# Kernel optimization log

Hardware: AMD Instinct MI355X
Metric: run time of the kernel (lower is better)

Reference implementation:

```python
import jax, jax.numpy as jnp
import numpy as np

N, E, F_DIM = 30000, 480000, 256
CLS_HID, NUM_CLASS, GEN_HID, MI_HID, BATCH = 128, 16, 64, 128, 4096
COM_L1, COM_L2, LAM, ALPHA, TAU, EPS = 0.5, 0.5, 0.5, 1.0, 0.5, 1e-8


def _glorot(key, shape):
    scale = jnp.sqrt(2.0 / (shape[0] + shape[-1]))
    return scale * jax.random.normal(key, shape, dtype=jnp.float32)


def setup_inputs() -> dict:
    key = jax.random.key(0)
    ks = jax.random.split(key, 32)
    inp = {
        'feat': jax.random.normal(ks[0], (N, F_DIM), dtype=jnp.float32),
        'view1_indices': jax.random.randint(ks[1], (2, E), 0, N),
        'view1_values': jax.random.uniform(ks[2], (E,), dtype=jnp.float32),
        'view2_indices': jax.random.randint(ks[3], (2, E), 0, N),
        'view2_values': jax.random.uniform(ks[4], (E,), dtype=jnp.float32),
        'idx': jnp.sort(jax.random.randint(ks[5], (BATCH,), 0, N)),
        # GenView (v1 and v2): gen_gcn weight + gen_mlp (Linear(2*gen_hid, 1))
        'W_gen_v1': _glorot(ks[6], (F_DIM, GEN_HID)),
        'Wm_v1': _glorot(ks[7], (2 * GEN_HID, 1)),
        'bm_v1': jnp.zeros((1,), dtype=jnp.float32),
        'W_gen_v2': _glorot(ks[8], (F_DIM, GEN_HID)),
        'Wm_v2': _glorot(ks[9], (2 * GEN_HID, 1)),
        'bm_v2': jnp.zeros((1,), dtype=jnp.float32),
        # Classification: three two-layer GCN encoders (v1, v2, v)
        'W1_v1': _glorot(ks[10], (F_DIM, CLS_HID)), 'W2_v1': _glorot(ks[11], (CLS_HID, NUM_CLASS)),
        'W1_v2': _glorot(ks[12], (F_DIM, CLS_HID)), 'W2_v2': _glorot(ks[13], (CLS_HID, NUM_CLASS)),
        'W1_v': _glorot(ks[14], (F_DIM, CLS_HID)), 'W2_v': _glorot(ks[15], (CLS_HID, NUM_CLASS)),
        # MI_NCE: three single GCN layers + shared projection MLP
        'Wg': _glorot(ks[16], (F_DIM, MI_HID)),
        'Wg1': _glorot(ks[17], (F_DIM, MI_HID)),
        'Wg2': _glorot(ks[18], (F_DIM, MI_HID)),
        'Wp1': _glorot(ks[19], (MI_HID, MI_HID)), 'bp1': jnp.zeros((MI_HID,), dtype=jnp.float32),
        'Wp2': _glorot(ks[20], (MI_HID, MI_HID)), 'bp2': jnp.zeros((MI_HID,), dtype=jnp.float32),
    }
    return inp


def spmm(idx, vals, x, n):
    # sparse COO adj (idx [2,E], vals [E]) @ dense x [n,d]
    return jax.ops.segment_sum(vals[:, None] * x[idx[1]], idx[0], num_segments=n)


def gcn_layer(x, idx, vals, W, n, act):
    h = spmm(idx, vals, x @ W, n)
    return jax.nn.relu(h) if act else h


def two_layer(x, idx, vals, W1, W2, n):
    return gcn_layer(gcn_layer(x, idx, vals, W1, n, True), idx, vals, W2, n, False)


def sparse_row_softmax(scores, rows, n):
    m = jax.lax.stop_gradient(jax.ops.segment_max(scores, rows, num_segments=n))
    e = jnp.exp(scores - m[rows])
    s = jax.ops.segment_sum(e, rows, num_segments=n)
    return e / s[rows]


def gen_view(feat, idx, vals, Wg, Wm, bm, com_lambda, n):
    emb = gcn_layer(feat, idx, vals, Wg, n, True)
    ff = jnp.concatenate([emb[idx[0]], emb[idx[1]]], axis=-1)  # [E, 2*gen_hid]
    temp = (ff @ Wm + bm).reshape(-1)
    pi = sparse_row_softmax(temp, idx[0], n)  # torch.sparse.softmax(dim=1)
    return vals + com_lambda * pi  # same sparsity pattern as v_ori


def sym(idx, vals):
    # normalize1 (big=True): adj + adj.T as COO concat (duplicates sum in spmm)
    return jnp.concatenate([idx, idx[::-1]], axis=1), jnp.concatenate([vals, vals])


def get_weight(prob):
    top2 = jax.lax.top_k(prob, 2)[0]
    fir, sec = top2[:, 0], top2[:, 1]
    return jnp.exp(ALPHA * (LAM * jnp.log(fir + EPS) + (1.0 - LAM) * jnp.log(fir - sec + EPS)))


def contrast_cal(z1, z2):
    num = z1 @ z2.T
    den = jnp.linalg.norm(z1, axis=-1, keepdims=True) @ jnp.linalg.norm(z2, axis=-1, keepdims=True).T
    m12 = jnp.exp(num / den / TAU)
    m21 = m12.T
    l12 = -jnp.log(jnp.diag(m12 / (m12.sum(1, keepdims=True) + EPS)) + EPS).mean()
    l21 = -jnp.log(jnp.diag(m21 / (m21.sum(1, keepdims=True) + EPS)) + EPS).mean()
    return 0.5 * (l12 + l21)


def cogsl_forward(feat, view1_values, view2_values,
                  W_gen_v1, Wm_v1, bm_v1, W_gen_v2, Wm_v2, bm_v2,
                  W1_v1, W2_v1, W1_v2, W2_v2, W1_v, W2_v,
                  Wg, Wg1, Wg2, Wp1, bp1, Wp2, bp2,
                  view1_indices, view2_indices, idx):
    n = feat.shape[0]
    # View_Estimator (GenView + normalize1)
    nv1 = gen_view(feat, view1_indices, view1_values, W_gen_v1, Wm_v1, bm_v1, COM_L1, n)
    nv2 = gen_view(feat, view2_indices, view2_values, W_gen_v2, Wm_v2, bm_v2, COM_L2, n)
    i1, v1 = sym(view1_indices, nv1)
    i2, v2 = sym(view2_indices, nv2)
    # Classification on each generated view
    prob_v1 = jax.nn.softmax(two_layer(feat, i1, v1, W1_v1, W2_v1, n), axis=1)
    prob_v2 = jax.nn.softmax(two_layer(feat, i2, v2, W1_v2, W2_v2, n), axis=1)
    logits_v1 = jnp.log(prob_v1 + EPS)
    logits_v2 = jnp.log(prob_v2 + EPS)
    # Fusion: per-node convex combination of the two sparse views (row scaling)
    w1 = get_weight(prob_v1)
    w2 = get_weight(prob_v2)
    b1 = w1 / (w1 + w2)
    b2 = w2 / (w1 + w2)
    idx_f = jnp.concatenate([i1, i2], axis=1)
    vals_f = jnp.concatenate([b1[i1[0]] * v1, b2[i2[0]] * v2])
    prob_v = jax.nn.softmax(two_layer(feat, idx_f, vals_f, W1_v, W2_v, n), axis=1)
    logits_v = jnp.log(prob_v + EPS)
    # MI_NCE over [fused v, v1, v2], big=True -> sample `batch` nodes
    proj = lambda h: jax.nn.elu(h @ Wp1 + bp1) @ Wp2 + bp2
    ev = proj(gcn_layer(feat, idx_f, vals_f, Wg, n, True))[idx]
    e1 = proj(gcn_layer(feat, i1, v1, Wg1, n, True))[idx]
    e2 = proj(gcn_layer(feat, i2, v2, Wg2, n, True))[idx]
    vv1 = contrast_cal(ev, e1)
    vv2 = contrast_cal(ev, e2)
    v1v2 = contrast_cal(e1, e2)
    return jnp.concatenate([logits_v.ravel(), logits_v1.ravel(), logits_v2.ravel(),
                            jnp.stack([vv1, vv2, v1v2])])


def reference(feat, view1_indices, view1_values, view2_indices, view2_values, idx,
              W_gen_v1, Wm_v1, bm_v1, W_gen_v2, Wm_v2, bm_v2,
              W1_v1, W2_v1, W1_v2, W2_v2, W1_v, W2_v,
              Wg, Wg1, Wg2, Wp1, bp1, Wp2, bp2):
    return cogsl_forward(feat, view1_values, view2_values,
                         W_gen_v1, Wm_v1, bm_v1, W_gen_v2, Wm_v2, bm_v2,
                         W1_v1, W2_v1, W1_v2, W2_v2, W1_v, W2_v,
                         Wg, Wg1, Wg2, Wp1, bp1, Wp2, bp2,
                         view1_indices, view2_indices, idx)
```

## Files before the change

### kernel.cpp

```cpp
#include <hip/hip_runtime.h>
#include <math.h>

#define NN 30000
#define EE 480000
#define FD 256
#define CH 128
#define NCLS 16
#define GH 64
#define MH 128
#define BT 4096
#define EPSc 1e-8f
#define GBc ((NN + 127) / 128)
#define SPB8 ((NN + 7) / 8)
#define SPB16 ((NN + 15) / 16)
#define RBc ((BT + 15) / 16)
#define PRB ((NN + 63) / 64)
#define PJB (BT / 8)
#define PX4 1056
#define SXB 1410
#define S64B ((NN + 15) / 16)

typedef __attribute__((ext_vector_type(8))) short short8;
typedef __attribute__((ext_vector_type(4))) float f32x4;

__device__ __forceinline__ unsigned short f2bf(float x) {
    unsigned b = __float_as_uint(x);
    unsigned r = b + 0x7FFFu + ((b >> 16) & 1u);
    return (unsigned short)(r >> 16);
}
__device__ __forceinline__ float bf2f(unsigned short h) {
    return __uint_as_float(((unsigned)h) << 16);
}
__device__ __forceinline__ float4 fma4(float s, float4 x, float4 a) {
    a.x = fmaf(s, x.x, a.x); a.y = fmaf(s, x.y, a.y);
    a.z = fmaf(s, x.z, a.z); a.w = fmaf(s, x.w, a.w);
    return a;
}

struct WSArgs {
    const float* s[8];
    unsigned short* h[8];
    unsigned short* l[8];
};

__global__ __launch_bounds__(256) void prep_all(
    const float* __restrict__ feat, unsigned short* __restrict__ fhi,
    unsigned short* __restrict__ flo, WSArgs a,
    const int* __restrict__ i1, const int* __restrict__ i2, int* __restrict__ cnt,
    int* __restrict__ sd1, int* __restrict__ sd2,
    int* __restrict__ sc1, int* __restrict__ sc2)
{
    int b = blockIdx.x;
    if (b < 30000) {
        long i = (long)b * 256 + threadIdx.x;
        float v = feat[i];
        unsigned short h = f2bf(v);
        fhi[i] = h;
        flo[i] = f2bf(v - bf2f(h));
        return;
    }
    b -= 30000;
    if (b < 896) {
        int i = b * 256 + threadIdx.x;
        if (i >= 229376) return;
        constexpr int NNp[8] = {64, 64, 128, 128, 128, 128, 128, 128};
        constexpr int OFF[9] = {0, 16384, 32768, 65536, 98304, 131072, 163840, 196608, 229376};
        int w = 0;
#pragma unroll
        for (int t = 1; t < 8; t++) if (i >= OFF[t]) w = t;
        int j = i - OFF[w];
        int N = NNp[w];
        int k = j / N, n = j % N;
        float v = a.s[w][j];
        unsigned short hh = f2bf(v);
        a.h[w][(size_t)n * 256 + k] = hh;
        a.l[w][(size_t)n * 256 + k] = f2bf(v - bf2f(hh));
        return;
    }
    b -= 896;
    int e = b * 256 + threadIdx.x;
    if (e >= EE) return;
    int r1 = i1[e], c1 = i1[EE + e];
    int r2 = i2[e], c2 = i2[EE + e];
    sd1[e] = atomicAdd(&cnt[r1], 1);
    sd2[e] = atomicAdd(&cnt[NN + r2], 1);
    sc1[e] = atomicAdd(&cnt[2 * NN + c1], 1);
    sc2[e] = atomicAdd(&cnt[3 * NN + c2], 1);
}

template <int NT, bool OUT16>
__device__ __forceinline__ void gemm3_body(
    unsigned short* sm, int bx,
    const unsigned short* __restrict__ Ahi, const unsigned short* __restrict__ Alo,
    const unsigned short* __restrict__ BThi, const unsigned short* __restrict__ BTlo,
    int K, void* __restrict__ Cv, int Cstride, int M)
{
    unsigned short* Ah = sm;
    unsigned short* Al = Ah + 128 * 40;
    unsigned short* Bh = Al + 128 * 40;
    unsigned short* Bl = Bh + NT * 16 * 40;
    int t = threadIdx.x;
    int w = t >> 6, l = t & 63;
    int lane = l & 15, quad = l >> 4;
    int row0 = bx * 128;
    f32x4 acc[2][NT];
#pragma unroll
    for (int s = 0; s < 2; s++)
#pragma unroll
        for (int n = 0; n < NT; n++) acc[s][n] = (f32x4)(0.f);

    int ar = t >> 1, ako = (t & 1) << 4;
    int nkc = K >> 5;
    for (int kc = 0; kc < nkc; kc++) {
        int kb = kc << 5;
        {
            int gr = row0 + ar;
            float4 h0, h1, l0, l1;
            if (gr < M) {
                const float4* pH = (const float4*)&Ahi[(size_t)gr * K + kb + ako];
                const float4* pL = (const float4*)&Alo[(size_t)gr * K + kb + ako];
                h0 = pH[0]; h1 = pH[1]; l0 = pL[0]; l1 = pL[1];
            } else {
                h0 = h1 = l0 = l1 = make_float4(0.f, 0.f, 0.f, 0.f);
            }
            float4* dH = (float4*)&Ah[ar * 40 + ako];
            dH[0] = h0; dH[1] = h1;
            float4* dL = (float4*)&Al[ar * 40 + ako];
            dL[0] = l0; dL[1] = l1;
        }
        if (ar < NT * 16) {
            const float4* pH = (const float4*)&BThi[(size_t)ar * K + kb + ako];
            const float4* pL = (const float4*)&BTlo[(size_t)ar * K + kb + ako];
            float4 h0 = pH[0], h1 = pH[1], l0 = pL[0], l1 = pL[1];
            float4* dH = (float4*)&Bh[ar * 40 + ako];
            dH[0] = h0; dH[1] = h1;
            float4* dL = (float4*)&Bl[ar * 40 + ako];
            dL[0] = l0; dL[1] = l1;
        }
        __syncthreads();
        short8 aH[2], aL[2];
#pragma unroll
        for (int s = 0; s < 2; s++) {
            int r = w * 32 + s * 16 + lane;
            aH[s] = *(const short8*)&Ah[r * 40 + quad * 8];
            aL[s] = *(const short8*)&Al[r * 40 + quad * 8];
        }
#pragma unroll
        for (int n = 0; n < NT; n++) {
            int r = n * 16 + lane;
            short8 bH = *(const short8*)&Bh[r * 40 + quad * 8];
            short8 bL = *(const short8*)&Bl[r * 40 + quad * 8];
#pragma unroll
            for (int s = 0; s < 2; s++) {
                acc[s][n] = __builtin_amdgcn_mfma_f32_16x16x32_bf16(aH[s], bH, acc[s][n], 0, 0, 0);
                acc[s][n] = __builtin_amdgcn_mfma_f32_16x16x32_bf16(aH[s], bL, acc[s][n], 0, 0, 0);
                acc[s][n] = __builtin_amdgcn_mfma_f32_16x16x32_bf16(aL[s], bH, acc[s][n], 0, 0, 0);
            }
        }
        __syncthreads();
    }
#pragma unroll
    for (int s = 0; s < 2; s++) {
        int rb = row0 + w * 32 + s * 16 + quad * 4;
#pragma unroll
        for (int reg = 0; reg < 4; reg++) {
            int gr = rb + reg;
            if (gr >= M) continue;
#pragma unroll
            for (int n = 0; n < NT; n++) {
                if (OUT16)
                    ((unsigned short*)Cv)[(size_t)gr * Cstride + n * 16 + lane] = f2bf(acc[s][n][reg]);
                else
                    ((float*)Cv)[(size_t)gr * Cstride + n * 16 + lane] = acc[s][n][reg];
            }
        }
    }
}

template <int NT, bool OUT16>
__device__ __forceinline__ void gemm1_body(
    unsigned short* sm, int bx,
    const unsigned short* __restrict__ Ahi,
    const unsigned short* __restrict__ BThi,
    int K, void* __restrict__ Cv, int Cstride, int M)
{
    unsigned short* Ah = sm;
    unsigned short* Bh = Ah + 128 * 40;
    int t = threadIdx.x;
    int w = t >> 6, l = t & 63;
    int lane = l & 15, quad = l >> 4;
    int row0 = bx * 128;
    f32x4 acc[2][NT];
#pragma unroll
    for (int s = 0; s < 2; s++)
#pragma unroll
        for (int n = 0; n < NT; n++) acc[s][n] = (f32x4)(0.f);

    int ar = t >> 1, ako = (t & 1) << 4;
    int nkc = K >> 5;
    for (int kc = 0; kc < nkc; kc++) {
        int kb = kc << 5;
        {
            int gr = row0 + ar;
            float4 h0, h1;
            if (gr < M) {
                const float4* pH = (const float4*)&Ahi[(size_t)gr * K + kb + ako];
                h0 = pH[0]; h1 = pH[1];
            } else {
                h0 = h1 = make_float4(0.f, 0.f, 0.f, 0.f);
            }
            float4* dH = (float4*)&Ah[ar * 40 + ako];
            dH[0] = h0; dH[1] = h1;
        }
        if (ar < NT * 16) {
            const float4* pH = (const float4*)&BThi[(size_t)ar * K + kb + ako];
            float4 h0 = pH[0], h1 = pH[1];
            float4* dH = (float4*)&Bh[ar * 40 + ako];
            dH[0] = h0; dH[1] = h1;
        }
        __syncthreads();
        short8 aH[2];
#pragma unroll
        for (int s = 0; s < 2; s++)
            aH[s] = *(const short8*)&Ah[(w * 32 + s * 16 + lane) * 40 + quad * 8];
#pragma unroll
        for (int n = 0; n < NT; n++) {
            short8 bH = *(const short8*)&Bh[(n * 16 + lane) * 40 + quad * 8];
#pragma unroll
            for (int s = 0; s < 2; s++)
                acc[s][n] = __builtin_amdgcn_mfma_f32_16x16x32_bf16(aH[s], bH, acc[s][n], 0, 0, 0);
        }
        __syncthreads();
    }
#pragma unroll
    for (int s = 0; s < 2; s++) {
        int rb = row0 + w * 32 + s * 16 + quad * 4;
#pragma unroll
        for (int reg = 0; reg < 4; reg++) {
            int gr = rb + reg;
            if (gr >= M) continue;
#pragma unroll
            for (int n = 0; n < NT; n++) {
                if (OUT16)
                    ((unsigned short*)Cv)[(size_t)gr * Cstride + n * 16 + lane] = f2bf(acc[s][n][reg]);
                else
                    ((float*)Cv)[(size_t)gr * Cstride + n * 16 + lane] = acc[s][n][reg];
            }
        }
    }
}

__global__ __launch_bounds__(256) void mega1a(
    const int* __restrict__ i1, const float* __restrict__ v1,
    const int* __restrict__ i2, const float* __restrict__ v2,
    const int* __restrict__ sd1, const int* __restrict__ sd2,
    const int* __restrict__ sc1, const int* __restrict__ sc2,
    const int* __restrict__ rp4,
    int2* __restrict__ ed1, int2* __restrict__ ec1,
    int2* __restrict__ ed2, int2* __restrict__ ec2,
    const unsigned short* __restrict__ feat_hi, const unsigned short* __restrict__ feat_lo,
    const unsigned short* __restrict__ wgen12h, const unsigned short* __restrict__ wgen12l,
    float* __restrict__ Pg)
{
    __shared__ unsigned short sm[128 * 40 * 2 + 8 * 16 * 40 * 2];
    int b = blockIdx.x;
    if (b < GBc) {
        gemm3_body<8, false>(sm, b, feat_hi, feat_lo, wgen12h, wgen12l, FD, Pg, 128, NN);
        return;
    }
    b -= GBc;
    int e = b * 256 + threadIdx.x;
    if (e >= EE) return;
    const int* rp_d1 = rp4;
    const int* rp_d2 = rp4 + (NN + 1);
    const int* rp_c1 = rp4 + 2 * (NN + 1);
    const int* rp_c2 = rp4 + 3 * (NN + 1);
    int r = i1[e], c = i1[EE + e];
    int p = rp_d1[r] + sd1[e];
    ed1[p] = make_int2(c, __float_as_int(v1[e]));
    ec1[rp_c1[c] + sc1[e]] = make_int2(r, p);
    r = i2[e]; c = i2[EE + e];
    p = rp_d2[r] + sd2[e];
    ed2[p] = make_int2(c, __float_as_int(v2[e]));
    ec2[rp_c2[c] + sc2[e]] = make_int2(r, p);
}

__global__ __launch_bounds__(1024) void scan_block4(const int* __restrict__ cnt,
                                                    int* __restrict__ rowptr,
                                                    int* __restrict__ bsum) {
    int y = blockIdx.y;
    int* rp = rowptr + y * (NN + 1);
    int* bs = bsum + y * 32;
    __shared__ int tmp[1024];
    int t = threadIdx.x;
    int i = blockIdx.x * 1024 + t;
    int v = (i < NN) ? cnt[y * NN + i] : 0;
    tmp[t] = v;
    __syncthreads();
    for (int off = 1; off < 1024; off <<= 1) {
        int add = (t >= off) ? tmp[t - off] : 0;
        __syncthreads();
        tmp[t] += add;
        __syncthreads();
    }
    if (i <= NN) rp[i] = tmp[t] - v;
    if (t == 1023) bs[blockIdx.x] = tmp[1023];
}
__global__ void scan_bsum4(int* __restrict__ bsum, int nb) {
    bsum += blockIdx.x * 32;
    int t = threadIdx.x;
    int orig = (t < nb) ? bsum[t] : 0;
    int v = orig;
    for (int off = 1; off < 64; off <<= 1) {
        int u = __shfl_up(v, off);
        if (t >= off) v += u;
    }
    if (t < nb) bsum[t] = v - orig;
}
__global__ void scan_add4(const int* __restrict__ bsum, int* __restrict__ rowptr) {
    int y = blockIdx.y;
    const int* bs = bsum + y * 32;
    int* rp = rowptr + y * (NN + 1);
    int i = blockIdx.x * 1024 + threadIdx.x;
    if (i <= NN) rp[i] += bs[blockIdx.x];
}

__global__ __launch_bounds__(256) void gen_nv(
    const int* __restrict__ rp_d, int2* __restrict__ ed1, int2* __restrict__ ed2,
    const float* __restrict__ sb, float* __restrict__ nvd1, float* __restrict__ nvd2)
{
    int y = blockIdx.y;
    int row = blockIdx.x * 256 + threadIdx.x;
    if (row >= NN) return;
    const int* rp = rp_d + y * (NN + 1);
    int2* ed = y ? ed2 : ed1;
    float* nvd = y ? nvd2 : nvd1;
    const float* sbv = sb + (size_t)y * NN;
    int p0 = rp[row], p1 = rp[row + 1];
    float m = -3.4e38f, sum = 0.f;
    for (int j = p0; j < p1; j += 8) {
        int cnt = p1 - j; if (cnt > 8) cnt = 8;
        float x[8];
#pragma unroll
        for (int e = 0; e < 8; e++)
            x[e] = (e < cnt) ? sbv[ed[j + e].x] : 0.f;
#pragma unroll
        for (int e = 0; e < 8; e++) {
            if (e < cnt) {
                float xx = x[e];
                if (xx > m) { sum = sum * expf(m - xx) + 1.f; m = xx; }
                else sum += expf(xx - m);
            }
        }
    }
    float inv = 1.f / sum;
    for (int j = p0; j < p1; j += 8) {
        int cnt = p1 - j; if (cnt > 8) cnt = 8;
        int2 q[8]; float x[8];
#pragma unroll
        for (int e = 0; e < 8; e++)
            q[e] = (e < cnt) ? ed[j + e] : make_int2(0, 0);
#pragma unroll
        for (int e = 0; e < 8; e++)
            x[e] = (e < cnt) ? sbv[q[e].x] : 0.f;
#pragma unroll
        for (int e = 0; e < 8; e++) {
            if (e < cnt) {
                float nv = __int_as_float(q[e].y) + 0.5f * expf(x[e] - m) * inv;
                nvd[j + e] = nv;
                ed[j + e].y = __float_as_int(nv);
            }
        }
    }
}

template <int STR4>
__device__ __forceinline__ void gath_dir_f32(
    const int* __restrict__ rp, const int2* __restrict__ ed, int row,
    const float4* __restrict__ x4, int xo, float4* a)
{
    int p0 = rp[row], p1 = rp[row + 1];
    int j = p0;
    for (; j + 8 <= p1; j += 8) {
        int2 q0 = ed[j], q1 = ed[j+1], q2 = ed[j+2], q3 = ed[j+3];
        int2 q4 = ed[j+4], q5 = ed[j+5], q6 = ed[j+6], q7 = ed[j+7];
        float4 x0 = x4[(size_t)q0.x * STR4 + xo];
        float4 x1 = x4[(size_t)q1.x * STR4 + xo];
        float4 x2 = x4[(size_t)q2.x * STR4 + xo];
        float4 x3 = x4[(size_t)q3.x * STR4 + xo];
        float4 x5 = x4[(size_t)q4.x * STR4 + xo];
        float4 x6 = x4[(size_t)q5.x * STR4 + xo];
        float4 x7 = x4[(size_t)q6.x * STR4 + xo];
        float4 x8 = x4[(size_t)q7.x * STR4 + xo];
        a[0] = fma4(__int_as_float(q0.y), x0, a[0]);
        a[1] = fma4(__int_as_float(q1.y), x1, a[1]);
        a[2] = fma4(__int_as_float(q2.y), x2, a[2]);
        a[3] = fma4(__int_as_float(q3.y), x3, a[3]);
        a[0] = fma4(__int_as_float(q4.y), x5, a[0]);
        a[1] = fma4(__int_as_float(q5.y), x6, a[1]);
        a[2] = fma4(__int_as_float(q6.y), x7, a[2]);
        a[3] = fma4(__int_as_float(q7.y), x8, a[3]);
    }
    for (; j + 4 <= p1; j += 4) {
        int2 q0 = ed[j], q1 = ed[j+1], q2 = ed[j+2], q3 = ed[j+3];
        a[0] = fma4(__int_as_float(q0.y), x4[(size_t)q0.x * STR4 + xo], a[0]);
        a[1] = fma4(__int_as_float(q1.y), x4[(size_t)q1.x * STR4 + xo], a[1]);
        a[2] = fma4(__int_as_float(q2.y), x4[(size_t)q2.x * STR4 + xo], a[2]);
        a[3] = fma4(__int_as_float(q3.y), x4[(size_t)q3.x * STR4 + xo], a[3]);
    }
    for (; j < p1; j++) {
        int2 q = ed[j];
        a[0] = fma4(__int_as_float(q.y), x4[(size_t)q.x * STR4 + xo], a[0]);
    }
}
template <int STR4>
__device__ __forceinline__ void gath_csc_f32(
    const int* __restrict__ rp, const int2* __restrict__ ec, const float* __restrict__ nvd,
    int row, const float4* __restrict__ x4, int xo, float4* a)
{
    int p0 = rp[row], p1 = rp[row + 1];
    int j = p0;
    for (; j + 8 <= p1; j += 8) {
        int2 q0 = ec[j], q1 = ec[j+1], q2 = ec[j+2], q3 = ec[j+3];
        int2 q4 = ec[j+4], q5 = ec[j+5], q6 = ec[j+6], q7 = ec[j+7];
        float4 x0 = x4[(size_t)q0.x * STR4 + xo];
        float4 x1 = x4[(size_t)q1.x * STR4 + xo];
        float4 x2 = x4[(size_t)q2.x * STR4 + xo];
        float4 x3 = x4[(size_t)q3.x * STR4 + xo];
        float4 x5 = x4[(size_t)q4.x * STR4 + xo];
        float4 x6 = x4[(size_t)q5.x * STR4 + xo];
        float4 x7 = x4[(size_t)q6.x * STR4 + xo];
        float4 x8 = x4[(size_t)q7.x * STR4 + xo];
        float v0 = nvd[q0.y], v1 = nvd[q1.y], v2 = nvd[q2.y], v3 = nvd[q3.y];
        float v4 = nvd[q4.y], v5 = nvd[q5.y], v6 = nvd[q6.y], v7 = nvd[q7.y];
        a[0] = fma4(v0, x0, a[0]);
        a[1] = fma4(v1, x1, a[1]);
        a[2] = fma4(v2, x2, a[2]);
        a[3] = fma4(v3, x3, a[3]);
        a[0] = fma4(v4, x5, a[0]);
        a[1] = fma4(v5, x6, a[1]);
        a[2] = fma4(v6, x7, a[2]);
        a[3] = fma4(v7, x8, a[3]);
    }
    for (; j + 4 <= p1; j += 4) {
        int2 q0 = ec[j], q1 = ec[j+1], q2 = ec[j+2], q3 = ec[j+3];
        float v0 = nvd[q0.y], v1 = nvd[q1.y], v2 = nvd[q2.y], v3 = nvd[q3.y];
        a[0] = fma4(v0, x4[(size_t)q0.x * STR4 + xo], a[0]);
        a[1] = fma4(v1, x4[(size_t)q1.x * STR4 + xo], a[1]);
        a[2] = fma4(v2, x4[(size_t)q2.x * STR4 + xo], a[2]);
        a[3] = fma4(v3, x4[(size_t)q3.x * STR4 + xo], a[3]);
    }
    for (; j < p1; j++) {
        int2 q = ec[j];
        a[0] = fma4(nvd[q.y], x4[(size_t)q.x * STR4 + xo], a[0]);
    }
}

__device__ __forceinline__ void spmm64_body(
    int y, int bx, const int* __restrict__ rp_d,
    const int2* __restrict__ e1, const int2* __restrict__ e2,
    const float* __restrict__ Pg, const float* __restrict__ Wm1,
    const float* __restrict__ Wm2, float* __restrict__ sb)
{
    const int* rp = rp_d + y * (NN + 1);
    const int2* arr = y ? e2 : e1;
    int row = bx * 16 + threadIdx.x / 16;
    int o = threadIdx.x % 16;
    if (row >= NN) return;
    float4 a[4] = {};
    gath_dir_f32<32>(rp, arr, row, (const float4*)Pg, y * 16 + o, a);
    float4 r;
    r.x = fmaxf((a[0].x + a[1].x) + (a[2].x + a[3].x), 0.f);
    r.y = fmaxf((a[0].y + a[1].y) + (a[2].y + a[3].y), 0.f);
    r.z = fmaxf((a[0].z + a[1].z) + (a[2].z + a[3].z), 0.f);
    r.w = fmaxf((a[0].w + a[1].w) + (a[2].w + a[3].w), 0.f);
    const float* Wmh = (y ? Wm2 : Wm1) + GH;
    float part = r.x * Wmh[o * 4] + r.y * Wmh[o * 4 + 1]
               + r.z * Wmh[o * 4 + 2] + r.w * Wmh[o * 4 + 3];
    part += __shfl_xor(part, 1); part += __shfl_xor(part, 2);
    part += __shfl_xor(part, 4); part += __shfl_xor(part, 8);
    if (o == 0) sb[y * NN + row] = part;
}

__global__ __launch_bounds__(256) void spmmX(
    const int* __restrict__ rp_d, const int2* __restrict__ ed1, const int2* __restrict__ ed2,
    const float* __restrict__ Pg, const float* __restrict__ Wm1,
    const float* __restrict__ Wm2, float* __restrict__ sb,
    const unsigned short* __restrict__ feat_hi, const unsigned short* __restrict__ feat_lo,
    const unsigned short* __restrict__ w1pairh, const unsigned short* __restrict__ w1pairl,
    float* __restrict__ P01,
    const unsigned short* __restrict__ w1vh, unsigned short* __restrict__ Ph2,
    const unsigned short* __restrict__ wgallh, unsigned short* __restrict__ Pmi16)
{
    __shared__ unsigned short sm[128 * 40 * 2 + 8 * 16 * 40 * 2];
    int b = blockIdx.x;
    int u = b >> 2, r = b & 3;
    if (r == 3) {
        if (u < 2 * GBc) {
            int y = u / GBc, bx = u % GBc;
            gemm3_body<8, false>(sm, bx, feat_hi, feat_lo,
                                 w1pairh + (size_t)y * 32768, w1pairl + (size_t)y * 32768,
                                 FD, P01 + (size_t)y * 128, 256, NN);
            return;
        }
        u -= 2 * GBc;
        if (u < GBc) {
            gemm1_body<8, true>(sm, u, feat_hi, w1vh, FD, Ph2, 128, NN);
            return;
        }
        u -= GBc;
        if (u < 3 * GBc) {
            int y = u / GBc, bx = u % GBc;
            gemm1_body<8, true>(sm, bx, feat_hi, wgallh + (size_t)y * 32768,
                                FD, Pmi16 + (size_t)y * 128, 384, NN);
        }
        return;
    }
    int s = u * 3 + r;
    if (s >= 2 * S64B) return;
    spmm64_body(s / S64B, s % S64B, rp_d, ed1, ed2, Pg, Wm1, Wm2, sb);
}

__device__ __forceinline__ void softmax16_epi(
    float4 r, int node, float* __restrict__ logits, float* __restrict__ wout)
{
    int o = threadIdx.x & 3;
    float mx = fmaxf(fmaxf(r.x, r.y), fmaxf(r.z, r.w));
    mx = fmaxf(mx, __shfl_xor(mx, 1));
    mx = fmaxf(mx, __shfl_xor(mx, 2));
    float e0 = expf(r.x - mx), e1 = expf(r.y - mx), e2 = expf(r.z - mx), e3 = expf(r.w - mx);
    float s = (e0 + e1) + (e2 + e3);
    s += __shfl_xor(s, 1);
    s += __shfl_xor(s, 2);
    float inv = 1.f / s;
    float p0 = e0 * inv, p1 = e1 * inv, p2 = e2 * inv, p3 = e3 * inv;
    float4 lg;
    lg.x = logf(p0 + EPSc); lg.y = logf(p1 + EPSc);
    lg.z = logf(p2 + EPSc); lg.w = logf(p3 + EPSc);
    ((float4*)logits)[(size_t)node * 4 + o] = lg;
    if (wout) {
        float f = p0, se = -1.f;
        if (p1 > f) { se = f; f = p1; } else se = p1;
        if (p2 > f) { se = f; f = p2; } else if (p2 > se) se = p2;
        if (p3 > f) { se = f; f = p3; } else if (p3 > se) se = p3;
#pragma unroll
        for (int d = 1; d <= 2; d <<= 1) {
            float of = __shfl_xor(f, d), os = __shfl_xor(se, d);
            if (of > f) { se = fmaxf(f, os); f = of; }
            else se = fmaxf(se, of);
        }
        if (o == 0)
            wout[node] = expf(0.5f * logf(f + EPSc) + 0.5f * logf(f - se + EPSc));
    }
}

__device__ __forceinline__ void pair_body(
    int y, int bx, const int* __restrict__ rp_d, const int* __restrict__ rp_c,
    const int2* __restrict__ ed1, const int2* __restrict__ ec1, const float* __restrict__ nvd1,
    const int2* __restrict__ ed2, const int2* __restrict__ ec2, const float* __restrict__ nvd2,
    const float* __restrict__ R01, float* __restrict__ logits_base, float* __restrict__ w12)
{
    const int* rpd = rp_d + y * (NN + 1);
    const int* rpc = rp_c + y * (NN + 1);
    const int2* ed = y ? ed2 : ed1;
    const int2* ec = y ? ec2 : ec1;
    const float* nvd = y ? nvd2 : nvd1;
    int row = bx * 64 + threadIdx.x / 4;
    int o = threadIdx.x % 4;
    if (row >= NN) return;
    const float4* x4 = (const float4*)(R01 + (size_t)y * NN * 16);
    float4 a[4] = {};
    gath_dir_f32<4>(rpd, ed, row, x4, o, a);
    gath_csc_f32<4>(rpc, ec, nvd, row, x4, o, a);
    float4 r;
    r.x = (a[0].x + a[1].x) + (a[2].x + a[3].x);
    r.y = (a[0].y + a[1].y) + (a[2].y + a[3].y);
    r.z = (a[0].z + a[1].z) + (a[2].z + a[3].z);
    r.w = (a[0].w + a[1].w) + (a[2].w + a[3].w);
    softmax16_epi(r, row, logits_base + (size_t)y * NN * NCLS, w12 + (size_t)y * NN);
}

__device__ __forceinline__ void fused_body(
    int bx, const int* __restrict__ rp_d, const int* __restrict__ rp_c,
    const int2* __restrict__ ed1, const int2* __restrict__ ec1, const float* __restrict__ nvd1,
    const int2* __restrict__ ed2, const int2* __restrict__ ec2, const float* __restrict__ nvd2,
    const float* __restrict__ w12, const float* __restrict__ x, float* __restrict__ logits)
{
    int row = bx * 64 + threadIdx.x / 4;
    int o = threadIdx.x % 4;
    if (row >= NN) return;
    const float4* x4 = (const float4*)x;
    float4 a[4] = {};
    gath_dir_f32<4>(rp_d, ed1, row, x4, o, a);
    gath_csc_f32<4>(rp_c, ec1, nvd1, row, x4, o, a);
    float4 s1;
    s1.x = (a[0].x + a[1].x) + (a[2].x + a[3].x);
    s1.y = (a[0].y + a[1].y) + (a[2].y + a[3].y);
    s1.z = (a[0].z + a[1].z) + (a[2].z + a[3].z);
    s1.w = (a[0].w + a[1].w) + (a[2].w + a[3].w);
    float4 b[4] = {};
    gath_dir_f32<4>(rp_d + (NN + 1), ed2, row, x4, o, b);
    gath_csc_f32<4>(rp_c + (NN + 1), ec2, nvd2, row, x4, o, b);
    float4 s2;
    s2.x = (b[0].x + b[1].x) + (b[2].x + b[3].x);
    s2.y = (b[0].y + b[1].y) + (b[2].y + b[3].y);
    s2.z = (b[0].z + b[1].z) + (b[2].z + b[3].z);
    s2.w = (b[0].w + b[1].w) + (b[2].w + b[3].w);
    float wa = w12[row], wb = w12[NN + row];
    float inv = 1.f / (wa + wb);
    float w1 = wa * inv, w2 = wb * inv;
    float4 r;
    r.x = w1 * s1.x + w2 * s2.x;
    r.y = w1 * s1.y + w2 * s2.y;
    r.z = w1 * s1.z + w2 * s2.z;
    r.w = w1 * s1.w + w2 * s2.w;
    softmax16_epi(r, row, logits, nullptr);
}

__device__ __forceinline__ void gath_dir_b16(
    const int* __restrict__ rp, const int2* __restrict__ ed, int row,
    const unsigned short* __restrict__ X, int xstride, int o, float* acc)
{
    int p0 = rp[row], p1 = rp[row + 1];
    int j = p0;
    for (; j + 8 <= p1; j += 8) {
        int2 q[8]; short8 x[8];
#pragma unroll
        for (int e = 0; e < 8; e++) q[e] = ed[j + e];
#pragma unroll
        for (int e = 0; e < 8; e++)
            x[e] = *(const short8*)&X[(size_t)q[e].x * xstride + o * 8];
#pragma unroll
        for (int e = 0; e < 8; e++) {
            float v = __int_as_float(q[e].y);
#pragma unroll
            for (int k = 0; k < 8; k++)
                acc[k] = fmaf(v, bf2f((unsigned short)x[e][k]), acc[k]);
        }
    }
    for (; j + 4 <= p1; j += 4) {
        int2 q0 = ed[j], q1 = ed[j+1], q2 = ed[j+2], q3 = ed[j+3];
        short8 x0 = *(const short8*)&X[(size_t)q0.x * xstride + o * 8];
        short8 x1 = *(const short8*)&X[(size_t)q1.x * xstride + o * 8];
        short8 x2 = *(const short8*)&X[(size_t)q2.x * xstride + o * 8];
        short8 x3 = *(const short8*)&X[(size_t)q3.x * xstride + o * 8];
        float v0 = __int_as_float(q0.y), v1 = __int_as_float(q1.y);
        float v2 = __int_as_float(q2.y), v3 = __int_as_float(q3.y);
#pragma unroll
        for (int k = 0; k < 8; k++) {
            acc[k] = fmaf(v0, bf2f((unsigned short)x0[k]), acc[k]);
            acc[k] = fmaf(v1, bf2f((unsigned short)x1[k]), acc[k]);
            acc[k] = fmaf(v2, bf2f((unsigned short)x2[k]), acc[k]);
            acc[k] = fmaf(v3, bf2f((unsigned short)x3[k]), acc[k]);
        }
    }
    for (; j < p1; j++) {
        int2 q = ed[j];
        short8 xv = *(const short8*)&X[(size_t)q.x * xstride + o * 8];
        float v = __int_as_float(q.y);
#pragma unroll
        for (int k = 0; k < 8; k++)
            acc[k] = fmaf(v, bf2f((unsigned short)xv[k]), acc[k]);
    }
}
__device__ __forceinline__ void gath_csc_b16(
    const int* __restrict__ rp, const int2* __restrict__ ec, const float* __restrict__ nvd,
    int row, const unsigned short* __restrict__ X, int xstride, int o, float* acc)
{
    int p0 = rp[row], p1 = rp[row + 1];
    int j = p0;
    for (; j + 8 <= p1; j += 8) {
        int2 q[8]; short8 x[8];
#pragma unroll
// ... 231 lines not shown
}

__device__ __forceinline__ void contrast_body(
    int p, int i0, int j0,
    const unsigned short* __restrict__ z16, float* __restrict__ stats, float* scol)
{
    int pa = (p == 2) ? 1 : 0;
    int pb = (p == 0) ? 1 : 2;
    const unsigned short* A = z16 + (size_t)pa * BT * MH;
    const unsigned short* B = z16 + (size_t)pb * BT * MH;
    float* diag = stats + (size_t)p * 3 * BT;
    float* rs = diag + BT;
    float* cs = rs + BT;
    int t = threadIdx.x;
    int w = t >> 6, l = t & 63, m = l & 15, quad = l >> 4;

    short8 afr[2][4];
#pragma unroll
    for (int s = 0; s < 2; s++) {
        const unsigned short* arow = &A[(size_t)(i0 + w * 32 + s * 16 + m) * MH + quad * 8];
#pragma unroll
        for (int kc = 0; kc < 4; kc++)
            afr[s][kc] = *(const short8*)(arow + kc * 32);
    }
    f32x4 acc[2][8];
#pragma unroll
    for (int s = 0; s < 2; s++)
#pragma unroll
        for (int n = 0; n < 8; n++) acc[s][n] = (f32x4)(0.f);

#pragma unroll
    for (int kc = 0; kc < 4; kc++) {
#pragma unroll
        for (int n = 0; n < 8; n++) {
            short8 bf = *(const short8*)&B[(size_t)(j0 + n * 16 + m) * MH + kc * 32 + quad * 8];
            acc[0][n] = __builtin_amdgcn_mfma_f32_16x16x32_bf16(afr[0][kc], bf, acc[0][n], 0, 0, 0);
            acc[1][n] = __builtin_amdgcn_mfma_f32_16x16x32_bf16(afr[1][kc], bf, acc[1][n], 0, 0, 0);
        }
    }
    float colp[8];
#pragma unroll
    for (int n = 0; n < 8; n++) colp[n] = 0.f;
#pragma unroll
    for (int s = 0; s < 2; s++) {
        int rbase = i0 + w * 32 + s * 16 + quad * 4;
#pragma unroll
        for (int reg = 0; reg < 4; reg++) {
            float rsum = 0.f;
            int gi = rbase + reg;
#pragma unroll
            for (int n = 0; n < 8; n++) {
                float mv = expf(acc[s][n][reg] * 2.0f);
                rsum += mv;
                colp[n] += mv;
                int gj = j0 + n * 16 + m;
                if (gi == gj) diag[gi] = mv;
            }
            rsum += __shfl_xor(rsum, 1); rsum += __shfl_xor(rsum, 2);
            rsum += __shfl_xor(rsum, 4); rsum += __shfl_xor(rsum, 8);
            if (m == 0) atomicAdd(&rs[gi], rsum);
        }
    }
    if (t < 128) scol[t] = 0.f;
    __syncthreads();
#pragma unroll
    for (int n = 0; n < 8; n++) {
        float v = colp[n];
        v += __shfl_xor(v, 16); v += __shfl_xor(v, 32);
        if (quad == (n & 3)) atomicAdd(&scol[n * 16 + m], v);
    }
    __syncthreads();
    if (t < 128) atomicAdd(&cs[j0 + t], scol[t]);
}

__global__ __launch_bounds__(256) void contrast_direct(
    const unsigned short* __restrict__ z16, float* __restrict__ stats)
{
    __shared__ float scol[128];
    contrast_body(blockIdx.z, blockIdx.y * 128, blockIdx.x * 128, z16, stats, scol);
}

__global__ __launch_bounds__(256) void pairX(
    const int* __restrict__ rp_d, const int* __restrict__ rp_c,
    const int2* __restrict__ ed1, const int2* __restrict__ ec1, const float* __restrict__ nvd1,
    const int2* __restrict__ ed2, const int2* __restrict__ ec2, const float* __restrict__ nvd2,
    const float* __restrict__ R01, float* __restrict__ logits_base, float* __restrict__ w12,
    const unsigned short* __restrict__ Ph2, float* __restrict__ A1, float* __restrict__ A2,
    const int* __restrict__ rows, const unsigned short* __restrict__ Pmi,
    float* __restrict__ G1, float* __restrict__ G2,
    const float* __restrict__ zQ,
    const float* __restrict__ Wp1, const float* __restrict__ bp1,
    const float* __restrict__ Wp2, const float* __restrict__ bp2,
    unsigned short* __restrict__ z16)
{
    __shared__ float psm[2064];
    int b = blockIdx.x;
    int u = b >> 2, r = b & 3;
    if (r == 0) {
        if (u < 2 * PRB)
            pair_body(u / PRB, u % PRB, rp_d, rp_c, ed1, ec1, nvd1, ed2, ec2, nvd2,
                      R01, logits_base, w12);
        return;
    }
    int idx = u * 3 + (r - 1);
    if (idx < SPB16) {
        b2gather_body(idx, rp_d, rp_c, ed1, ec1, nvd1, ed2, ec2, nvd2, Ph2, A1, A2);
        return;
    }
    idx -= SPB16;
    if (idx < RBc) {
        rows0_gather_body(idx, rp_d, rp_c, ed1, ec1, nvd1, ed2, ec2, nvd2,
                          rows, Pmi, G1, G2);
        return;
    }
    idx -= RBc;
    if (idx < 2 * PJB) {
        int plane = 1 + idx / PJB;
        proj8_body(psm, psm + 1024, psm + 2048, idx % PJB, plane,
                   zQ, Wp1, bp1, Wp2, bp2, z16);
    }
}

__global__ __launch_bounds__(256) void combineB2(
    const float* __restrict__ w12,
    const float* __restrict__ A1, const float* __restrict__ A2,
    const float* __restrict__ W2v, float* __restrict__ R2,
    const int* __restrict__ rows,
    const float* __restrict__ G1, const float* __restrict__ G2,
    float* __restrict__ zQ,
    const unsigned short* __restrict__ z16, float* __restrict__ stats)
{
    __shared__ float sm[2048 + 16 * 128];
    int b = blockIdx.x;
    int r = threadIdx.x / 16;
    int o = threadIdx.x % 16;
    if (b < SPB16) {
        float* W2s = sm;
        float* Qs  = sm + 2048;
        for (int i = threadIdx.x; i < 2048; i += 256) W2s[i] = W2v[i];
        int row = b * 16 + r;
        float wa = w12[row], wb = w12[NN + row];
        float inv = 1.f / (wa + wb);
        float w1 = wa * inv, w2 = wb * inv;
        const float* p1 = A1 + (size_t)row * 128 + o * 8;
        const float* p2 = A2 + (size_t)row * 128 + o * 8;
#pragma unroll
        for (int k = 0; k < 8; k++)
            Qs[r * 128 + o * 8 + k] = fmaxf(w1 * p1[k] + w2 * p2[k], 0.f);
        __syncthreads();
        int t = threadIdx.x;
        int rr = t >> 4, c = t & 15;
        int grow = b * 16 + rr;
        float acc = 0.f;
        const float* qrow = &sm[2048 + rr * 128];
#pragma unroll 8
        for (int k = 0; k < 128; k++)
            acc = fmaf(qrow[k], sm[k * 16 + c], acc);
        R2[(size_t)grow * 16 + c] = acc;
        return;
    }
    b -= SPB16;
    if (b < RBc) {
        int ri = b * 16 + r;
        if (ri >= BT) return;
        int node = rows[ri];
        float wa = w12[node], wb = w12[NN + node];
        float inv = 1.f / (wa + wb);
        float w1 = wa * inv, w2 = wb * inv;
        const float* p1 = G1 + (size_t)ri * 128 + o * 8;
        const float* p2 = G2 + (size_t)ri * 128 + o * 8;
        float* out = zQ + (size_t)ri * 128 + o * 8;
#pragma unroll
        for (int k = 0; k < 8; k++)
            out[k] = fmaxf(w1 * p1[k] + w2 * p2[k], 0.f);
        return;
    }
    b -= RBc;
    contrast_body(2, (b >> 5) * 128, (b & 31) * 128, z16, stats, sm);
}

__global__ __launch_bounds__(256) void fusedX(
    const int* __restrict__ rp_d, const int* __restrict__ rp_c,
    const int2* __restrict__ ed1, const int2* __restrict__ ec1, const float* __restrict__ nvd1,
    const int2* __restrict__ ed2, const int2* __restrict__ ec2, const float* __restrict__ nvd2,
    const float* __restrict__ w12, const float* __restrict__ R2, float* __restrict__ logits,
    const float* __restrict__ zQ,
    const float* __restrict__ Wp1, const float* __restrict__ bp1,
    const float* __restrict__ Wp2, const float* __restrict__ bp2,
    unsigned short* __restrict__ z16)
{
    __shared__ float psm[2064];
    int b = blockIdx.x;
    if (b < PRB) {
        fused_body(b, rp_d, rp_c, ed1, ec1, nvd1, ed2, ec2, nvd2, w12, R2, logits);
        return;
    }
    proj8_body(psm, psm + 1024, psm + 2048, b - PRB, 0, zQ, Wp1, bp1, Wp2, bp2, z16);
}

__global__ void contrast_reduce(const float* __restrict__ stats, float* __restrict__ out3)
{
    int p = blockIdx.x, t = threadIdx.x;
    const float* diag = stats + (size_t)p * 3 * BT;
    const float* rs = diag + BT;
    const float* cs = rs + BT;
    float s1 = 0.f, s2 = 0.f;
    for (int i = t; i < BT; i += 256) {
        float d = diag[i];
        s1 += logf(d / (rs[i] + EPSc) + EPSc);
        s2 += logf(d / (cs[i] + EPSc) + EPSc);
    }
#pragma unroll
    for (int off = 32; off; off >>= 1) { s1 += __shfl_down(s1, off); s2 += __shfl_down(s2, off); }
    __shared__ float sh[8];
    if ((t & 63) == 0) { sh[(t >> 6) * 2] = s1; sh[(t >> 6) * 2 + 1] = s2; }
    __syncthreads();
    if (t == 0) {
        float a = sh[0] + sh[2] + sh[4] + sh[6];
        float b = sh[1] + sh[3] + sh[5] + sh[7];
        out3[p] = 0.5f * (-a / BT - b / BT);
    }
}

extern "C" void kernel_launch(void* const* d_in, const int* in_sizes, int n_in,
                              void* d_out, int out_size, void* d_ws, size_t ws_size,
                              hipStream_t stream)
{
    const float* feat   = (const float*)d_in[0];
    const int*   ind1   = (const int*)d_in[1];
    const float* vals1  = (const float*)d_in[2];
    const int*   ind2   = (const int*)d_in[3];
    const float* vals2  = (const float*)d_in[4];
    const int*   idxb   = (const int*)d_in[5];
    const float* Wm1    = (const float*)d_in[7];
    const float* Wm2    = (const float*)d_in[10];
    const float* W2_v1  = (const float*)d_in[13];
    const float* W2_v2  = (const float*)d_in[15];
    const float* W2_v   = (const float*)d_in[17];
    const float* Wp1    = (const float*)d_in[21];
    const float* bp1    = (const float*)d_in[22];
    const float* Wp2    = (const float*)d_in[23];
    const float* bp2    = (const float*)d_in[24];
    float* dout = (float*)d_out;

    float* ws = (float*)d_ws;
    size_t off = 0;
    auto alloc = [&](size_t n) { n = (n + 3) & ~(size_t)3; float* p = ws + off; off += n; return p; };
    auto alloc_s = [&](size_t n) { return (unsigned short*)alloc((n + 1) / 2); };

    float* pool = alloc(16000000);
    float* Pg   = pool;
    float* P01  = pool + 3840000;
    float* R01  = pool + 11520000;
    float* zQ   = pool + 12480000;
    float* A1   = pool;
    float* G1   = pool + 14052864;
    float* G2   = pool + 14577152;
    float* R2   = pool + 15101440;

    unsigned short* feat_hi = alloc_s((size_t)NN * FD);
    unsigned short* feat_lo = alloc_s((size_t)NN * FD);
    float* A2 = (float*)feat_hi;
    unsigned short* Ph2d    = alloc_s((size_t)NN * CH);
    unsigned short* Pmi16d  = alloc_s((size_t)NN * 384);
    float* sb   = alloc(2 * NN);
    float* w12  = alloc(2 * NN);
    float* stats = alloc((size_t)3 * 3 * BT);
    unsigned short* z16 = alloc_s((size_t)3 * BT * MH);
    int2* ed1 = (int2*)alloc(2 * (size_t)EE);
    int2* ed2 = (int2*)alloc(2 * (size_t)EE);
    int2* ec1 = (int2*)alloc(2 * (size_t)EE);
    int2* ec2 = (int2*)alloc(2 * (size_t)EE);
    float* nvd1 = alloc(EE);
    float* nvd2 = alloc(EE);
    int* sd1 = (int*)alloc(EE);
    int* sd2 = (int*)alloc(EE);
    int* sc1 = (int*)alloc(EE);
    int* sc2 = (int*)alloc(EE);
    int* rp4  = (int*)alloc(4 * (NN + 1));
    int* cnt4 = (int*)alloc(4 * NN);
    int* bsum = (int*)alloc(128);
    int* rp_d = rp4;
    int* rp_c = rp4 + 2 * (NN + 1);
    unsigned short* wgen12h = alloc_s(32768); unsigned short* wgen12l = alloc_s(32768);
    unsigned short* w1pairh = alloc_s(65536); unsigned short* w1pairl = alloc_s(65536);
    unsigned short* w1vh    = alloc_s(32768); unsigned short* w1vl    = alloc_s(32768);
    unsigned short* wgallh  = alloc_s(98304); unsigned short* wgalll  = alloc_s(98304);

    const int NB = (NN + 1 + 1023) / 1024;
    const int NCNT = (EE + 255) / 256;

    hipMemsetAsync(cnt4, 0, 4 * NN * 4, stream);
    WSArgs a;
    a.s[0] = (const float*)d_in[6];  a.h[0] = wgen12h;          a.l[0] = wgen12l;
    a.s[1] = (const float*)d_in[9];  a.h[1] = wgen12h + 16384;  a.l[1] = wgen12l + 16384;
    a.s[2] = (const float*)d_in[12]; a.h[2] = w1pairh;          a.l[2] = w1pairl;
    a.s[3] = (const float*)d_in[14]; a.h[3] = w1pairh + 32768;  a.l[3] = w1pairl + 32768;
    a.s[4] = (const float*)d_in[16]; a.h[4] = w1vh;             a.l[4] = w1vl;
    a.s[5] = (const float*)d_in[18]; a.h[5] = wgallh;           a.l[5] = wgalll;
    a.s[6] = (const float*)d_in[19]; a.h[6] = wgallh + 32768;   a.l[6] = wgalll + 32768;
    a.s[7] = (const float*)d_in[20]; a.h[7] = wgallh + 65536;   a.l[7] = wgalll + 65536;
    prep_all<<<30000 + 896 + NCNT, 256, 0, stream>>>(feat, feat_hi, feat_lo, a,
                                                     ind1, ind2, cnt4, sd1, sd2, sc1, sc2);

    scan_block4<<<dim3(NB, 4), 1024, 0, stream>>>(cnt4, rp4, bsum);
    scan_bsum4<<<4, 64, 0, stream>>>(bsum, NB);
    scan_add4<<<dim3(NB, 4), 1024, 0, stream>>>(bsum, rp4);

    mega1a<<<GBc + NCNT, 256, 0, stream>>>(ind1, vals1, ind2, vals2,
                                           sd1, sd2, sc1, sc2, rp4,
                                           ed1, ec1, ed2, ec2,
                                           feat_hi, feat_lo, wgen12h, wgen12l, Pg);

    spmmX<<<4 * SXB, 256, 0, stream>>>(rp_d, ed1, ed2, Pg, Wm1, Wm2, sb,
                                       feat_hi, feat_lo, w1pairh, w1pairl, P01,
                                       w1vh, Ph2d, wgallh, Pmi16d);

    gen_nv<<<dim3((NN + 255) / 256, 2), 256, 0, stream>>>(rp_d, ed1, ed2, sb, nvd1, nvd2);
    hipMemsetAsync(stats, 0, (size_t)3 * 3 * BT * 4, stream);

    mega2<<<2 * SPB8 + 2 * RBc, 256, 0, stream>>>(rp_d, rp_c, ed1, ec1, nvd1,
                                                  ed2, ec2, nvd2, P01, W2_v1, W2_v2,
                                                  R01, idxb, Pmi16d, zQ);

    pairX<<<4 * PX4, 256, 0, stream>>>(rp_d, rp_c, ed1, ec1, nvd1, ed2, ec2, nvd2,
                                       R01, dout + (size_t)NN * NCLS, w12,
                                       Ph2d, A1, A2, idxb, Pmi16d, G1, G2,
                                       zQ, Wp1, bp1, Wp2, bp2, z16);

    combineB2<<<SPB16 + RBc + 1024, 256, 0, stream>>>(w12, A1, A2, W2_v, R2, idxb,
                                                      G1, G2, zQ, z16, stats);

    fusedX<<<PRB + PJB, 256, 0, stream>>>(rp_d, rp_c, ed1, ec1, nvd1, ed2, ec2, nvd2,
                                          w12, R2, dout, zQ, Wp1, bp1, Wp2, bp2, z16);

    contrast_direct<<<dim3(32, 32, 2), 256, 0, stream>>>(z16, stats);
    contrast_reduce<<<3, 256, 0, stream>>>(stats, dout + (size_t)3 * NN * NCLS);
}
```

Measured before the change: 840.7 us.

## Move feature GEMMs into edge-scatter kernel and split score SpMM into own launch

The six feature-projection GEMM tiles that were interleaved with the score SpMM blocks in spmmX now run in the mega1x launch, alongside the generator GEMM and the CSR edge scatter. The score SpMM becomes a standalone kernel with a 2D grid. The aim is to overlap the compute-heavy GEMMs with the memory-bound edge scatter instead of with the gather SpMM, and to free the SpMM from the interleaved block-index mapping. This makes the first kernel larger and leaves the SpMM as a separate, purely memory-bound launch. The combine kernel's shared-memory accesses are also renamed to use named Qs/W2s pointers.

```diff
diff --git a/kernel.cpp b/kernel.cpp
--- a/kernel.cpp
+++ b/kernel.cpp
@@ -17,8 +17,6 @@
 #define PRB ((NN + 63) / 64)
 #define PJB (BT / 8)
 #define PX4 1056
-#define SXB 1410
-#define S64B ((NN + 15) / 16)
 
 typedef __attribute__((ext_vector_type(8))) short short8;
 typedef __attribute__((ext_vector_type(4))) float f32x4;
@@ -250,7 +248,7 @@
     }
 }
 
-__global__ __launch_bounds__(256) void mega1a(
+__global__ __launch_bounds__(256) void mega1x(
     const int* __restrict__ i1, const float* __restrict__ v1,
     const int* __restrict__ i2, const float* __restrict__ v2,
     const int* __restrict__ sd1, const int* __restrict__ sd2,
@@ -260,7 +258,11 @@
     int2* __restrict__ ed2, int2* __restrict__ ec2,
     const unsigned short* __restrict__ feat_hi, const unsigned short* __restrict__ feat_lo,
     const unsigned short* __restrict__ wgen12h, const unsigned short* __restrict__ wgen12l,
-    float* __restrict__ Pg)
+    float* __restrict__ Pg,
+    const unsigned short* __restrict__ w1pairh, const unsigned short* __restrict__ w1pairl,
+    float* __restrict__ P01,
+    const unsigned short* __restrict__ w1vh, unsigned short* __restrict__ Ph2,
+    const unsigned short* __restrict__ wgallh, unsigned short* __restrict__ Pmi16)
 {
     __shared__ unsigned short sm[128 * 40 * 2 + 8 * 16 * 40 * 2];
     int b = blockIdx.x;
@@ -269,6 +271,26 @@
         return;
     }
     b -= GBc;
+    if (b < 2 * GBc) {
+        int y = b / GBc, bx = b % GBc;
+        gemm3_body<8, false>(sm, bx, feat_hi, feat_lo,
+                             w1pairh + (size_t)y * 32768, w1pairl + (size_t)y * 32768,
+                             FD, P01 + (size_t)y * 128, 256, NN);
+        return;
+    }
+    b -= 2 * GBc;
+    if (b < GBc) {
+        gemm1_body<8, true>(sm, b, feat_hi, w1vh, FD, Ph2, 128, NN);
+        return;
+    }
+    b -= GBc;
+    if (b < 3 * GBc) {
+        int y = b / GBc, bx = b % GBc;
+        gemm1_body<8, true>(sm, bx, feat_hi, wgallh + (size_t)y * 32768,
+                            FD, Pmi16 + (size_t)y * 128, 384, NN);
+        return;
+    }
+    b -= 3 * GBc;
     int e = b * 256 + threadIdx.x;
     if (e >= EE) return;
     const int* rp_d1 = rp4;
@@ -456,15 +478,15 @@
     }
 }
 
-__device__ __forceinline__ void spmm64_body(
-    int y, int bx, const int* __restrict__ rp_d,
-    const int2* __restrict__ e1, const int2* __restrict__ e2,
+__global__ __launch_bounds__(256) void spmm64_scores(
+    const int* __restrict__ rp_d, const int2* __restrict__ e1, const int2* __restrict__ e2,
     const float* __restrict__ Pg, const float* __restrict__ Wm1,
     const float* __restrict__ Wm2, float* __restrict__ sb)
 {
+    int y = blockIdx.y;
     const int* rp = rp_d + y * (NN + 1);
     const int2* arr = y ? e2 : e1;
-    int row = bx * 16 + threadIdx.x / 16;
+    int row = blockIdx.x * 16 + threadIdx.x / 16;
     int o = threadIdx.x % 16;
     if (row >= NN) return;
     float4 a[4] = {};
@@ -480,45 +502,6 @@
     part += __shfl_xor(part, 1); part += __shfl_xor(part, 2);
     part += __shfl_xor(part, 4); part += __shfl_xor(part, 8);
     if (o == 0) sb[y * NN + row] = part;
-}
-
-__global__ __launch_bounds__(256) void spmmX(
-    const int* __restrict__ rp_d, const int2* __restrict__ ed1, const int2* __restrict__ ed2,
-    const float* __restrict__ Pg, const float* __restrict__ Wm1,
-    const float* __restrict__ Wm2, float* __restrict__ sb,
-    const unsigned short* __restrict__ feat_hi, const unsigned short* __restrict__ feat_lo,
-    const unsigned short* __restrict__ w1pairh, const unsigned short* __restrict__ w1pairl,
-    float* __restrict__ P01,
-    const unsigned short* __restrict__ w1vh, unsigned short* __restrict__ Ph2,
-    const unsigned short* __restrict__ wgallh, unsigned short* __restrict__ Pmi16)
-{
-    __shared__ unsigned short sm[128 * 40 * 2 + 8 * 16 * 40 * 2];
-    int b = blockIdx.x;
-    int u = b >> 2, r = b & 3;
-    if (r == 3) {
-        if (u < 2 * GBc) {
-            int y = u / GBc, bx = u % GBc;
-            gemm3_body<8, false>(sm, bx, feat_hi, feat_lo,
-                                 w1pairh + (size_t)y * 32768, w1pairl + (size_t)y * 32768,
-                                 FD, P01 + (size_t)y * 128, 256, NN);
-            return;
-        }
-        u -= 2 * GBc;
-        if (u < GBc) {
-            gemm1_body<8, true>(sm, u, feat_hi, w1vh, FD, Ph2, 128, NN);
-            return;
-        }
-        u -= GBc;
-        if (u < 3 * GBc) {
-            int y = u / GBc, bx = u % GBc;
-            gemm1_body<8, true>(sm, bx, feat_hi, wgallh + (size_t)y * 32768,
-                                FD, Pmi16 + (size_t)y * 128, 384, NN);
-        }
-        return;
-    }
-    int s = u * 3 + r;
-    if (s >= 2 * S64B) return;
-    spmm64_body(s / S64B, s % S64B, rp_d, ed1, ed2, Pg, Wm1, Wm2, sb);
 }
 
 __device__ __forceinline__ void softmax16_epi(
@@ -1056,10 +1039,10 @@
         int rr = t >> 4, c = t & 15;
         int grow = b * 16 + rr;
         float acc = 0.f;
-        const float* qrow = &sm[2048 + rr * 128];
+        const float* qrow = &Qs[rr * 128];
 #pragma unroll 8
         for (int k = 0; k < 128; k++)
-            acc = fmaf(qrow[k], sm[k * 16 + c], acc);
+            acc = fmaf(qrow[k], W2s[k * 16 + c], acc);
         R2[(size_t)grow * 16 + c] = acc;
         return;
     }
@@ -1211,15 +1194,14 @@
     scan_bsum4<<<4, 64, 0, stream>>>(bsum, NB);
     scan_add4<<<dim3(NB, 4), 1024, 0, stream>>>(bsum, rp4);
 
-    mega1a<<<GBc + NCNT, 256, 0, stream>>>(ind1, vals1, ind2, vals2,
-                                           sd1, sd2, sc1, sc2, rp4,
-                                           ed1, ec1, ed2, ec2,
-                                           feat_hi, feat_lo, wgen12h, wgen12l, Pg);
-
-    spmmX<<<4 * SXB, 256, 0, stream>>>(rp_d, ed1, ed2, Pg, Wm1, Wm2, sb,
-                                       feat_hi, feat_lo, w1pairh, w1pairl, P01,
-                                       w1vh, Ph2d, wgallh, Pmi16d);
-
+    mega1x<<<7 * GBc + NCNT, 256, 0, stream>>>(ind1, vals1, ind2, vals2,
+                                               sd1, sd2, sc1, sc2, rp4,
+                                               ed1, ec1, ed2, ec2,
+                                               feat_hi, feat_lo, wgen12h, wgen12l, Pg,
+                                               w1pairh, w1pairl, P01,
+                                               w1vh, Ph2d, wgallh, Pmi16d);
+
+    spmm64_scores<<<dim3((NN + 15) / 16, 2), 256, 0, stream>>>(rp_d, ed1, ed2, Pg, Wm1, Wm2, sb);
     gen_nv<<<dim3((NN + 255) / 256, 2), 256, 0, stream>>>(rp_d, ed1, ed2, sb, nvd1, nvd2);
     hipMemsetAsync(stats, 0, (size_t)3 * 3 * BT * 4, stream);
 
```

Result: faster. 774.6 us (-7.9%).
